# Kernel optimization log

Hardware: AMD Instinct MI355X
Metric: run time of the kernel (lower is better)

Reference implementation:

```python
import jax, jax.numpy as jnp
import numpy as np

B, N, D, E, H = 8, 2048, 256, 16, 8
CAP = max(min(N, int(N * 2.0 / E)), 4)  # eval capacity_factor = 2.0 -> 256
EPS = 1e-9
LOSS_COEF = 0.01


def _excl_cumsum(t, axis):
    return jnp.cumsum(t, axis=axis) - t


def _top2_gating(x, w_gating):
    # x: (B, N, D); w_gating: (D, E)
    raw = jax.nn.softmax(jnp.einsum('bnd,de->bne', x, w_gating), axis=-1)
    idx1 = jnp.argmax(raw, axis=-1)
    g1 = jnp.max(raw, axis=-1)
    m1 = jax.nn.one_hot(idx1, E, dtype=raw.dtype)
    gates2 = raw * (1.0 - m1)
    idx2 = jnp.argmax(gates2, axis=-1)
    g2 = jnp.max(gates2, axis=-1)
    m2 = jax.nn.one_hot(idx2, E, dtype=raw.dtype)
    denom = g1 + g2 + EPS
    g1 = g1 / denom
    g2 = g2 / denom
    # load-balance loss
    density_1 = m1.mean(axis=-2)          # (B, E)
    proxy = raw.mean(axis=-2)             # (B, E)
    loss = (proxy * density_1).mean() * float(E * E)
    # second policy == 'all': keep mask_2 as-is
    pos1 = _excl_cumsum(m1, -2) * m1
    m1 = m1 * (pos1 < float(CAP)).astype(m1.dtype)
    m1_count = m1.sum(axis=-2, keepdims=True)
    m1_flat = m1.sum(axis=-1)             # (B, N)
    pos1 = pos1.sum(axis=-1)              # (B, N)
    g1 = g1 * m1_flat
    pos2 = (_excl_cumsum(m2, -2) + m1_count) * m2
    m2 = m2 * (pos2 < float(CAP)).astype(m2.dtype)
    m2_flat = m2.sum(axis=-1)
    pos2 = pos2.sum(axis=-1)
    g2 = g2 * m2_flat
    oh_e1 = jax.nn.one_hot(idx1, E, dtype=raw.dtype)
    oh_e2 = jax.nn.one_hot(idx2, E, dtype=raw.dtype)
    oh_c1 = jax.nn.one_hot(pos1.astype(jnp.int32), CAP, dtype=raw.dtype)
    oh_c2 = jax.nn.one_hot(pos2.astype(jnp.int32), CAP, dtype=raw.dtype)
    # combine: (B, N, E, CAP); note torch applies mask_flat twice (idempotent)
    combine = ((g1 * m1_flat)[..., None, None] * oh_e1[..., :, None] * oh_c1[..., None, :]
               + (g2 * m2_flat)[..., None, None] * oh_e2[..., :, None] * oh_c2[..., None, :])
    dispatch = (combine > 0).astype(combine.dtype)
    return dispatch, combine, loss


def _mixer(xe, audio, Wq, Wkv, Wp, bp):
    # CrossModalMixer, eval mode (dropouts = identity)
    # xe: (B, CAP, D); audio: (B, 1, D)
    b, n, c = xe.shape
    dh = c // H
    scale = dh ** -0.5
    q = (audio @ Wq).reshape(b, 1, H, dh).transpose(0, 2, 1, 3)   # (b,h,1,dh)
    kv = (xe @ Wkv).reshape(b, n, 2, H, dh)
    k = kv[:, :, 0].transpose(0, 2, 1, 3)                          # (b,h,n,dh)
    v = kv[:, :, 1].transpose(0, 2, 1, 3)
    attn = jax.nn.softmax(jnp.einsum('bhqd,bhkd->bhqk', q, k) * scale, axis=-1)
    o = jnp.einsum('bhqk,bhkd->bhqd', attn, v).transpose(0, 2, 1, 3).reshape(b, 1, c)
    gate = jax.nn.sigmoid(o @ Wp + bp)                             # (b,1,c)
    return xe * gate                                               # einsum('bnc,bc->bnc')


def setup_inputs():
    ks = jax.random.split(jax.random.key(0), 7)
    return {
        'x': jax.random.normal(ks[0], (B, N, D), jnp.float32),
        'audio_feat': jax.random.normal(ks[1], (B, 1, D), jnp.float32),
        'w_gating': jax.random.normal(ks[2], (D, E), jnp.float32),
        'Wq': jax.random.normal(ks[3], (E, D, D), jnp.float32) * 0.02,
        'Wkv': jax.random.normal(ks[4], (E, D, 2 * D), jnp.float32) * 0.02,
        'Wp': jax.random.normal(ks[5], (E, D, D), jnp.float32) * 0.02,
        'bp': jnp.zeros((E, D), jnp.float32),
    }


def reference(x, audio_feat, w_gating, Wq, Wkv, Wp, bp):
    dispatch, combine, loss = _top2_gating(x, w_gating)
    expert_in = jnp.einsum('bnd,bnec->ebcd', x, dispatch)          # (E, B, CAP, D)
    outs = jax.vmap(_mixer, in_axes=(0, None, 0, 0, 0, 0))(expert_in, audio_feat, Wq, Wkv, Wp, bp)
    out = jnp.einsum('ebcd,bnec->bnd', outs, combine)
    return out, loss * LOSS_COEF
```

## Files before the change

### kernel.cpp

```cpp
#include <hip/hip_runtime.h>
#include <cstdint>
#include <cstddef>

#define BB 8
#define NN 2048
#define DD 256
#define EE 16
#define HH 8
#define CAPC 256
#define BN (BB*NN)
#define EB (EE*BB)

__global__ __launch_bounds__(256) void fused_gq_kernel(
    const float* __restrict__ x, const float* __restrict__ wg,
    const float* __restrict__ audio, const float* __restrict__ Wq,
    const float* __restrict__ Wkv,
    int* __restrict__ idx1a, int* __restrict__ idx2a,
    float* __restrict__ g1a, float* __restrict__ g2a,
    float* __restrict__ raw_part, float* __restrict__ cnt_part,
    float* __restrict__ rws)
{
  __shared__ union SM {
    struct { float wgS[DD*EE]; float lgp[4][64][17]; } g;
    struct { float aS[DD][8]; float qpart[8][32][9]; float qS[32][8];
             float wkS[DD][33]; } q;
  } sm;
  int tid = threadIdx.x;

  if (blockIdx.x < 256) {
    for (int t = tid; t < DD*EE; t += 256) sm.g.wgS[t] = wg[t];
    __syncthreads();
    int tk = tid & 63, kc = tid >> 6;
    int token0 = blockIdx.x * 64;
    int token = token0 + tk;
    const float4* xr = (const float4*)(x + (size_t)token*DD + kc*64);
    const float4* wg4 = (const float4*)sm.g.wgS;
    float lg[16];
#pragma unroll
    for (int e = 0; e < 16; ++e) lg[e] = 0.f;
#pragma unroll
    for (int d4 = 0; d4 < 16; ++d4) {
      float4 xv = xr[d4];
      float xa[4] = {xv.x, xv.y, xv.z, xv.w};
#pragma unroll
      for (int dd = 0; dd < 4; ++dd) {
        int d = kc*64 + d4*4 + dd;
        float xc = xa[dd];
#pragma unroll
        for (int j = 0; j < 4; ++j) {
          float4 w = wg4[d*4 + j];
          lg[4*j+0] += xc*w.x; lg[4*j+1] += xc*w.y;
          lg[4*j+2] += xc*w.z; lg[4*j+3] += xc*w.w;
        }
      }
    }
#pragma unroll
    for (int e = 0; e < 16; ++e) sm.g.lgp[kc][tk][e] = lg[e];
    __syncthreads();
    if (tid < 64) {
      int lane = tid;
      float l[16];
#pragma unroll
      for (int e = 0; e < 16; ++e)
        l[e] = sm.g.lgp[0][lane][e] + sm.g.lgp[1][lane][e]
             + sm.g.lgp[2][lane][e] + sm.g.lgp[3][lane][e];
      float mx = l[0];
#pragma unroll
      for (int e = 1; e < 16; ++e) mx = fmaxf(mx, l[e]);
      float p[16]; float s = 0.f;
#pragma unroll
      for (int e = 0; e < 16; ++e) { p[e] = expf(l[e] - mx); s += p[e]; }
      int i1 = 0; float b1 = p[0];
#pragma unroll
      for (int e = 1; e < 16; ++e) { if (p[e] > b1) { b1 = p[e]; i1 = e; } }
      float b2 = (i1 == 0) ? 0.f : p[0]; int i2 = 0;
#pragma unroll
      for (int e = 1; e < 16; ++e) { float v = (e == i1) ? 0.f : p[e]; if (v > b2) { b2 = v; i2 = e; } }
      float inv = 1.f / s;
      float g1 = b1*inv, g2 = b2*inv;
      float den = g1 + g2 + 1e-9f;
      g1 /= den; g2 /= den;
      int tok = token0 + lane;
      idx1a[tok] = i1; idx2a[tok] = i2;
      g1a[tok] = g1;   g2a[tok] = g2;
      int blk = blockIdx.x;
#pragma unroll
      for (int e = 0; e < 16; ++e) {
        float v = p[e] * inv;
        v += __shfl_down(v, 32); v += __shfl_down(v, 16);
        v += __shfl_down(v, 8);  v += __shfl_down(v, 4);
        v += __shfl_down(v, 2);  v += __shfl_down(v, 1);
        unsigned long long mb = __ballot(i1 == e);
        if (lane == 0) {
          raw_part[blk*16 + e] = v;
          cnt_part[blk*16 + e] = (float)__popcll(mb);
        }
      }
    }
  } else {
    int eh = blockIdx.x - 256;
    int e = eh >> 3, h = eh & 7;
    for (int i = tid; i < 2048; i += 256) { int b = i >> 8, k = i & 255; sm.q.aS[k][b] = audio[b*DD + k]; }
    __syncthreads();
    int j = tid & 31, kg = tid >> 5;
    const float* wq = Wq + (size_t)e*DD*DD + h*32 + j;
    float acc[8] = {0,0,0,0,0,0,0,0};
#pragma unroll
    for (int i = 0; i < 32; ++i) {
      int k = kg*32 + i;
      float w = wq[(size_t)k*DD];
      float4 a0 = *(const float4*)&sm.q.aS[k][0];
      float4 a1 = *(const float4*)&sm.q.aS[k][4];
      acc[0]+=w*a0.x; acc[1]+=w*a0.y; acc[2]+=w*a0.z; acc[3]+=w*a0.w;
      acc[4]+=w*a1.x; acc[5]+=w*a1.y; acc[6]+=w*a1.z; acc[7]+=w*a1.w;
    }
#pragma unroll
    for (int b = 0; b < 8; ++b) sm.q.qpart[kg][j][b] = acc[b];
    const float* wkbase = Wkv + (size_t)e*(DD*2*DD) + h*32;
    float4 stg[8];
#pragma unroll
    for (int m = 0; m < 8; ++m) {
      int row = m*32 + (tid >> 3), c4 = tid & 7;
      stg[m] = *(const float4*)(wkbase + (size_t)row*(2*DD) + c4*4);
    }
#pragma unroll
    for (int m = 0; m < 8; ++m) {
      int row = m*32 + (tid >> 3), c4 = tid & 7;
      sm.q.wkS[row][c4*4+0] = stg[m].x; sm.q.wkS[row][c4*4+1] = stg[m].y;
      sm.q.wkS[row][c4*4+2] = stg[m].z; sm.q.wkS[row][c4*4+3] = stg[m].w;
    }
    __syncthreads();
    {
      int jj = tid >> 3, b = tid & 7;
      float s = 0.f;
#pragma unroll
      for (int g = 0; g < 8; ++g) s += sm.q.qpart[g][jj][b];
      sm.q.qS[jj][b] = s;
    }
    __syncthreads();
    int d = tid;
    float racc[8] = {0,0,0,0,0,0,0,0};
#pragma unroll
    for (int jj = 0; jj < 32; ++jj) {
      float w = sm.q.wkS[d][jj];
      float4 q0 = *(const float4*)&sm.q.qS[jj][0];
      float4 q1 = *(const float4*)&sm.q.qS[jj][4];
      racc[0]+=w*q0.x; racc[1]+=w*q0.y; racc[2]+=w*q0.z; racc[3]+=w*q0.w;
      racc[4]+=w*q1.x; racc[5]+=w*q1.y; racc[6]+=w*q1.z; racc[7]+=w*q1.w;
    }
#pragma unroll
    for (int b = 0; b < 8; ++b)
      rws[((size_t)(e*8 + b))*2048 + d*8 + h] = racc[b];
  }
}

__global__ __launch_bounds__(256) void scan_kernel(
    const int* __restrict__ idx1a, const int* __restrict__ idx2a,
    float* __restrict__ g1a, float* __restrict__ g2a, int* __restrict__ slot_token,
    const float* __restrict__ raw_part, const float* __restrict__ cnt_part,
    float* __restrict__ out_loss)
{
  __shared__ unsigned long long m1s[16][32], m2s[16][32];
  __shared__ int wp1[16][32], wp2[16][32], mcnt[16];
  int b = blockIdx.x, tid = threadIdx.x;
  int wave = tid >> 6, lane = tid & 63;
  for (int i = tid; i < 16*CAPC; i += 256) {
    int e = i >> 8, s = i & 255;
    slot_token[(e*BB + b)*CAPC + s] = -1;
  }
  for (int w = wave; w < 32; w += 4) {
    int token = b*NN + w*64 + lane;
    int i1 = idx1a[token], i2 = idx2a[token];
#pragma unroll
    for (int e = 0; e < 16; ++e) {
      unsigned long long ma = __ballot(i1 == e);
      unsigned long long mb = __ballot(i2 == e);
      if (lane == 0) { m1s[e][w] = ma; m2s[e][w] = mb; }
    }
  }
  __syncthreads();
  if (tid < 16) {
    int run = 0;
    for (int w = 0; w < 32; ++w) { wp1[tid][w] = run; run += (int)__popcll(m1s[tid][w]); }
    mcnt[tid] = run < CAPC ? run : CAPC;
  } else if (tid < 32) {
    int e2 = tid - 16; int run = 0;
    for (int w = 0; w < 32; ++w) { wp2[e2][w] = run; run += (int)__popcll(m2s[e2][w]); }
  }
  __syncthreads();
  for (int w = wave; w < 32; w += 4) {
    int token = b*NN + w*64 + lane;
    int i1 = idx1a[token], i2 = idx2a[token];
    unsigned long long lt = (1ull << lane) - 1ull;
    int pos1 = wp1[i1][w] + (int)__popcll(m1s[i1][w] & lt);
    float g1 = g1a[token];
    bool k1 = pos1 < CAPC;
    g1a[token] = k1 ? g1 : 0.f;
    if (k1) slot_token[(i1*BB + b)*CAPC + pos1] = token;
    int pos2 = mcnt[i2] + wp2[i2][w] + (int)__popcll(m2s[i2][w] & lt);
    float g2 = g2a[token];
    bool k2 = pos2 < CAPC;
    g2a[token] = k2 ? g2 : 0.f;
    if (k2 && g2 > 0.f) slot_token[(i2*BB + b)*CAPC + pos2] = token;
  }
  if (blockIdx.x == 0) {
    float v = 0.f;
    if (tid < 128) {
      int bb = tid >> 4, e = tid & 15;
      float rs = 0.f, cs = 0.f;
#pragma unroll 4
      for (int k = 0; k < 32; ++k) {
        rs += raw_part[(bb*32 + k)*16 + e];
        cs += cnt_part[(bb*32 + k)*16 + e];
      }
      v = (rs * (1.f/(float)NN)) * (cs * (1.f/(float)NN));
    }
    v += __shfl_down(v, 32); v += __shfl_down(v, 16); v += __shfl_down(v, 8);
    v += __shfl_down(v, 4);  v += __shfl_down(v, 2);  v += __shfl_down(v, 1);
    __shared__ float r4[4];
    if ((tid & 63) == 0) r4[tid >> 6] = v;
    __syncthreads();
    if (tid == 0)
      out_loss[0] = (r4[0]+r4[1]+r4[2]+r4[3]) * ((float)(EE*EE) / (float)(BB*EE)) * 0.01f;
  }
}

__global__ __launch_bounds__(256) void lslotB_kernel(
    const float* __restrict__ x, const float* __restrict__ rws,
    const int* __restrict__ slot_token, float* __restrict__ lslot)
{
  __shared__ float rS[DD][8];
  __shared__ float lp[4][64][9];
  __shared__ int tokS[64];
  int tid = threadIdx.x;
  int eb = blockIdx.x >> 2, sc = blockIdx.x & 3;
  {
    const float4* rin = (const float4*)(rws + (size_t)eb*2048);
    float4* rS4 = (float4*)rS;
    rS4[tid] = rin[tid]; rS4[tid+256] = rin[tid+256];
  }
  if (tid < 64) tokS[tid] = slot_token[eb*CAPC + sc*64 + tid];
  __syncthreads();
  int s = tid >> 2, q = tid & 3;
  int token = tokS[s];
  float l[8] = {0,0,0,0,0,0,0,0};
  if (token >= 0) {
    const float4* xr = (const float4*)(x + (size_t)token*DD + q*64);
#pragma unroll
    for (int i = 0; i < 16; ++i) {
      float4 xv = xr[i];
      float xa[4] = {xv.x, xv.y, xv.z, xv.w};
#pragma unroll
      for (int dd = 0; dd < 4; ++dd) {
        int d = q*64 + i*4 + dd;
        float4 r0 = *(const float4*)&rS[d][0];
        float4 r1 = *(const float4*)&rS[d][4];
        float xc = xa[dd];
        l[0]+=xc*r0.x; l[1]+=xc*r0.y; l[2]+=xc*r0.z; l[3]+=xc*r0.w;
        l[4]+=xc*r1.x; l[5]+=xc*r1.y; l[6]+=xc*r1.z; l[7]+=xc*r1.w;
      }
    }
  }
#pragma unroll
  for (int h = 0; h < 8; ++h) lp[q][s][h] = l[h];
  __syncthreads();
#pragma unroll
  for (int r = 0; r < 2; ++r) {
    int o = tid*2 + r;
    int ss = o >> 3, h = o & 7;
    float v = (lp[0][ss][h] + lp[1][ss][h] + lp[2][ss][h] + lp[3][ss][h])
            * 0.17677669529663687f;
    lslot[((size_t)eb*CAPC + sc*64 + ss)*8 + h] = v;
  }
}

__global__ __launch_bounds__(256) void xattn_kernel(
    const float* __restrict__ x, const float* __restrict__ lslot,
    const int* __restrict__ slot_token, float* __restrict__ xattn)
{
  __shared__ float lS[CAPC][9];
  __shared__ float aS[HH][CAPC];
  __shared__ float part[4][HH][64];
  __shared__ int tokS[CAPC];
  __shared__ float red[16];
  int tid = threadIdx.x;
  int eb = blockIdx.x >> 2, dc = blockIdx.x & 3;
  int d0 = dc*64;
  {
    const float4* li = (const float4*)(lslot + (size_t)eb*CAPC*8);
    float4 v0 = li[tid*2], v1 = li[tid*2+1];
    lS[tid][0]=v0.x; lS[tid][1]=v0.y; lS[tid][2]=v0.z; lS[tid][3]=v0.w;
    lS[tid][4]=v1.x; lS[tid][5]=v1.y; lS[tid][6]=v1.z; lS[tid][7]=v1.w;
    tokS[tid] = slot_token[eb*CAPC + tid];
  }
  __syncthreads();
  int lane = tid & 63, wave = tid >> 6;
#pragma unroll
  for (int r = 0; r < 2; ++r) {
    int hh = wave + r*4;
    float m = fmaxf(fmaxf(lS[lane][hh], lS[lane+64][hh]),
                    fmaxf(lS[lane+128][hh], lS[lane+192][hh]));
    m = fmaxf(m, __shfl_down(m,32)); m = fmaxf(m, __shfl_down(m,16));
    m = fmaxf(m, __shfl_down(m,8));  m = fmaxf(m, __shfl_down(m,4));
    m = fmaxf(m, __shfl_down(m,2));  m = fmaxf(m, __shfl_down(m,1));
    if (lane == 0) red[hh] = m;
  }
  __syncthreads();
  float ex[8];
#pragma unroll
  for (int h = 0; h < 8; ++h) { ex[h] = expf(lS[tid][h] - red[h]); lS[tid][h] = ex[h]; }
  __syncthreads();
#pragma unroll
  for (int r = 0; r < 2; ++r) {
    int hh = wave + r*4;
    float s = lS[lane][hh] + lS[lane+64][hh] + lS[lane+128][hh] + lS[lane+192][hh];
    s += __shfl_down(s,32); s += __shfl_down(s,16); s += __shfl_down(s,8);
    s += __shfl_down(s,4);  s += __shfl_down(s,2);  s += __shfl_down(s,1);
    if (lane == 0) red[8+hh] = s;
  }
  __syncthreads();
#pragma unroll
  for (int h = 0; h < 8; ++h) aS[h][tid] = ex[h] / red[8+h];
  __syncthreads();
  int d = tid & 63, sc = tid >> 6;
  const float* xb = x + d0 + d;
  float acc[8] = {0,0,0,0,0,0,0,0};
#pragma unroll 4
  for (int i = 0; i < 64; ++i) {
    int s = sc*64 + i;
    int tk = tokS[s];
    int tkc = tk < 0 ? 0 : tk;
    float msk = tk < 0 ? 0.f : 1.f;
    float xv = xb[(size_t)tkc*DD] * msk;
#pragma unroll
    for (int h = 0; h < 8; ++h) acc[h] += aS[h][s] * xv;
  }
#pragma unroll
  for (int h = 0; h < 8; ++h) part[sc][h][d] = acc[h];
  __syncthreads();
#pragma unroll
  for (int r = 0; r < 2; ++r) {
    int o = r*256 + tid;
    int h = o >> 6, d2 = o & 63;
    float v = part[0][h][d2] + part[1][h][d2] + part[2][h][d2] + part[3][h][d2];
    xattn[(size_t)eb*2048 + h*DD + d0 + d2] = v;
  }
}

__global__ __launch_bounds__(256) void o_kernel(
    const float* __restrict__ xattn, const float* __restrict__ Wkv,
    float* __restrict__ o_ws)
{
  __shared__ float xaS[8][DD];
  __shared__ float op[8][32][9];
  int tid = threadIdx.x;
  int e = blockIdx.x >> 3, ch = blockIdx.x & 7;
  int c0 = ch*32, h = ch;
  for (int i = tid; i < 2048; i += 256) {
    int b = i >> 8, d = i & 255;
    xaS[b][d] = xattn[((size_t)(e*8 + b))*2048 + h*DD + d];
  }
  __syncthreads();
  int c = tid & 31, kc = tid >> 5;
  const float* wv = Wkv + (size_t)e*(DD*2*DD) + DD + c0 + c;
  float acc[8] = {0,0,0,0,0,0,0,0};
#pragma unroll
  for (int i = 0; i < 32; ++i) {
    int d = kc*32 + i;
    float w = wv[(size_t)d*(2*DD)];
#pragma unroll
    for (int b = 0; b < 8; ++b) acc[b] += w * xaS[b][d];
  }
#pragma unroll
  for (int b = 0; b < 8; ++b) op[kc][c][b] = acc[b];
  __syncthreads();
  int c2 = tid & 31, b2 = tid >> 5;
  float s = 0.f;
#pragma unroll
  for (int g = 0; g < 8; ++g) s += op[g][c2][b2];
  o_ws[((size_t)(e*8 + b2))*DD + c0 + c2] = s;
}

__global__ __launch_bounds__(256) void gate_kernel(
    const float* __restrict__ o_ws, const float* __restrict__ Wp,
    const float* __restrict__ bp, float* __restrict__ gateW)
{
  __shared__ float oS[8][DD];
  __shared__ float op[8][32][9];
  int tid = threadIdx.x;
  int e = blockIdx.x >> 3, ch = blockIdx.x & 7;
  int c0 = ch*32;
  for (int i = tid; i < 2048; i += 256) {
    int b = i >> 8, d = i & 255;
    oS[b][d] = o_ws[((size_t)(e*8 + b))*DD + d];
  }
  __syncthreads();
  int c = tid & 31, kc = tid >> 5;
  const float* wp = Wp + (size_t)e*DD*DD + c0 + c;
  float acc[8] = {0,0,0,0,0,0,0,0};
#pragma unroll
  for (int i = 0; i < 32; ++i) {
    int d = kc*32 + i;
    float w = wp[(size_t)d*DD];
#pragma unroll
    for (int b = 0; b < 8; ++b) acc[b] += w * oS[b][d];
  }
#pragma unroll
  for (int b = 0; b < 8; ++b) op[kc][c][b] = acc[b];
  __syncthreads();
  int c2 = tid & 31, b2 = tid >> 5;
  float s = bp[e*DD + c0 + c2];
#pragma unroll
  for (int g = 0; g < 8; ++g) s += op[g][c2][b2];
  gateW[((size_t)(e*8 + b2))*DD + c0 + c2] = 1.f / (1.f + expf(-s));
}

__global__ __launch_bounds__(256) void out_kernel(
    const float* __restrict__ x, const float* __restrict__ g1f, const float* __restrict__ g2f,
    const int* __restrict__ idx1a, const int* __restrict__ idx2a,
    const float* __restrict__ gateW, float* __restrict__ out)
{
  int idx = blockIdx.x*256 + threadIdx.x;
  int token = idx >> 6;
  int d4 = idx & 63;
  int b = token >> 11;
  float g1 = g1f[token], g2 = g2f[token];
  int e1 = idx1a[token], e2 = idx2a[token];
  float4 w1 = ((const float4*)(gateW + (size_t)(e1*BB+b)*DD))[d4];
  float4 w2 = ((const float4*)(gateW + (size_t)(e2*BB+b)*DD))[d4];
  float4 xv = ((const float4*)x)[idx];
  float4 o;
  o.x = xv.x*(g1*w1.x + g2*w2.x);
  o.y = xv.y*(g1*w1.y + g2*w2.y);
  o.z = xv.z*(g1*w1.z + g2*w2.z);
  o.w = xv.w*(g1*w1.w + g2*w2.w);
  ((float4*)out)[idx] = o;
}

extern "C" void kernel_launch(void* const* d_in, const int* in_sizes, int n_in,
                              void* d_out, int out_size, void* d_ws, size_t ws_size,
                              hipStream_t stream)
{
  const float* x     = (const float*)d_in[0];
  const float* audio = (const float*)d_in[1];
  const float* wg    = (const float*)d_in[2];
  const float* Wq    = (const float*)d_in[3];
  const float* Wkv   = (const float*)d_in[4];
  const float* Wp    = (const float*)d_in[5];
  const float* bp    = (const float*)d_in[6];
  float* out = (float*)d_out;

  float* raw_part = (float*)d_ws;
  float* cnt_part = raw_part + 256*16;
  int*   idx1a   = (int*)(cnt_part + 256*16);
  int*   idx2a   = idx1a + BN;
  float* g1a     = (float*)(idx2a + BN);
  float* g2a     = g1a + BN;
  int*   slot_token = (int*)(g2a + BN);
  float* rws     = (float*)(slot_token + EB*CAPC);
  float* lslot   = rws + (size_t)EB*2048;
  float* xattn   = lslot + (size_t)EB*CAPC*8;
  float* o_ws    = xattn + (size_t)EB*2048;
  float* gateW   = o_ws + (size_t)EB*DD;

  fused_gq_kernel<<<384, 256, 0, stream>>>(x, wg, audio, Wq, Wkv,
                                           idx1a, idx2a, g1a, g2a,
                                           raw_part, cnt_part, rws);
  scan_kernel<<<BB, 256, 0, stream>>>(idx1a, idx2a, g1a, g2a, slot_token,
                                      raw_part, cnt_part, out + (size_t)out_size - 1);
  lslotB_kernel<<<EB*4, 256, 0, stream>>>(x, rws, slot_token, lslot);
  xattn_kernel<<<EB*4, 256, 0, stream>>>(x, lslot, slot_token, xattn);
  o_kernel<<<EB, 256, 0, stream>>>(xattn, Wkv, o_ws);
  gate_kernel<<<EB, 256, 0, stream>>>(o_ws, Wp, bp, gateW);
  out_kernel<<<(BN*DD/4)/256, 256, 0, stream>>>(x, g1a, g2a, idx1a, idx2a, gateW, out);
}
```

Baseline: 155.6 us.

## Fuse per-expert attention, projection and gate kernels; prefetch weights during scan

Merges the four per-expert kernels (logit, attention-weighted sum, V projection, gate projection) into one 512-thread kernel per (expert,batch). The intermediate buffers and their global round trips go away, along with three launches. Extra blocks are added to the scan kernel that read all of Wkv and Wp to warm the cache while the scan runs. In exchange, the fused kernel launches only 128 blocks and each block now recomputes the V and Wp projections for a single batch. That multiplies weight reads by 8 compared with the earlier kernels, which shared each weight load across all 8 batches.

```diff
diff --git a/kernel.cpp b/kernel.cpp
--- a/kernel.cpp
+++ b/kernel.cpp
@@ -158,11 +158,26 @@
     const int* __restrict__ idx1a, const int* __restrict__ idx2a,
     float* __restrict__ g1a, float* __restrict__ g2a, int* __restrict__ slot_token,
     const float* __restrict__ raw_part, const float* __restrict__ cnt_part,
+    const float* __restrict__ Wkv, const float* __restrict__ Wp,
+    float* __restrict__ dummy,
     float* __restrict__ out_loss)
 {
+  int tid = threadIdx.x;
+  if (blockIdx.x >= BB) {
+    int pid = (blockIdx.x - BB)*256 + tid;
+    const float4* wk4 = (const float4*)Wkv;
+    const float4* wp4 = (const float4*)Wp;
+    float s = 0.f;
+    for (int i = pid; i < 786432; i += 56*256) {
+      float4 v = (i < 524288) ? wk4[i] : wp4[i - 524288];
+      s += v.x + v.y + v.z + v.w;
+    }
+    if (s != 0.f) dummy[pid & 1023] = s;
+    return;
+  }
   __shared__ unsigned long long m1s[16][32], m2s[16][32];
   __shared__ int wp1[16][32], wp2[16][32], mcnt[16];
-  int b = blockIdx.x, tid = threadIdx.x;
+  int b = blockIdx.x;
   int wave = tid >> 6, lane = tid & 63;
   for (int i = tid; i < 16*CAPC; i += 256) {
     int e = i >> 8, s = i & 255;
@@ -225,194 +240,145 @@
   }
 }
 
-__global__ __launch_bounds__(256) void lslotB_kernel(
+__global__ __launch_bounds__(512) void expert_kernel(
     const float* __restrict__ x, const float* __restrict__ rws,
-    const int* __restrict__ slot_token, float* __restrict__ lslot)
+    const int* __restrict__ slot_token, const float* __restrict__ Wkv,
+    const float* __restrict__ Wp, const float* __restrict__ bp,
+    float* __restrict__ gateW)
 {
   __shared__ float rS[DD][8];
-  __shared__ float lp[4][64][9];
-  __shared__ int tokS[64];
+  __shared__ int   tokS[CAPC];
+  __shared__ float lp[2][CAPC][9];
+  __shared__ float aST[CAPC][8];
+  __shared__ float part[2][8][DD];
+  __shared__ float xaS[8][DD];
+  __shared__ float oS[DD];
+  __shared__ float op[2][DD];
   int tid = threadIdx.x;
-  int eb = blockIdx.x >> 2, sc = blockIdx.x & 3;
+  int eb = blockIdx.x;
+  int e  = eb >> 3;
+
   {
     const float4* rin = (const float4*)(rws + (size_t)eb*2048);
-    float4* rS4 = (float4*)rS;
-    rS4[tid] = rin[tid]; rS4[tid+256] = rin[tid+256];
-  }
-  if (tid < 64) tokS[tid] = slot_token[eb*CAPC + sc*64 + tid];
-  __syncthreads();
-  int s = tid >> 2, q = tid & 3;
-  int token = tokS[s];
-  float l[8] = {0,0,0,0,0,0,0,0};
-  if (token >= 0) {
-    const float4* xr = (const float4*)(x + (size_t)token*DD + q*64);
-#pragma unroll
-    for (int i = 0; i < 16; ++i) {
-      float4 xv = xr[i];
-      float xa[4] = {xv.x, xv.y, xv.z, xv.w};
-#pragma unroll
-      for (int dd = 0; dd < 4; ++dd) {
-        int d = q*64 + i*4 + dd;
-        float4 r0 = *(const float4*)&rS[d][0];
-        float4 r1 = *(const float4*)&rS[d][4];
-        float xc = xa[dd];
-        l[0]+=xc*r0.x; l[1]+=xc*r0.y; l[2]+=xc*r0.z; l[3]+=xc*r0.w;
-        l[4]+=xc*r1.x; l[5]+=xc*r1.y; l[6]+=xc*r1.z; l[7]+=xc*r1.w;
+    ((float4*)rS)[tid] = rin[tid];
+    if (tid < CAPC) tokS[tid] = slot_token[eb*CAPC + tid];
+  }
+  __syncthreads();
+
+  {
+    int s = tid >> 1, q = tid & 1;
+    int token = tokS[s];
+    float l[8] = {0,0,0,0,0,0,0,0};
+    if (token >= 0) {
+      const float4* xr = (const float4*)(x + (size_t)token*DD) + q;
+#pragma unroll
+      for (int i = 0; i < 32; ++i) {
+        float4 xv = xr[i*2];
+        float xa[4] = {xv.x, xv.y, xv.z, xv.w};
+#pragma unroll
+        for (int dd = 0; dd < 4; ++dd) {
+          int d = i*8 + q*4 + dd;
+          float4 r0 = *(const float4*)&rS[d][0];
+          float4 r1 = *(const float4*)&rS[d][4];
+          float xc = xa[dd];
+          l[0]+=xc*r0.x; l[1]+=xc*r0.y; l[2]+=xc*r0.z; l[3]+=xc*r0.w;
+          l[4]+=xc*r1.x; l[5]+=xc*r1.y; l[6]+=xc*r1.z; l[7]+=xc*r1.w;
+        }
       }
     }
-  }
-#pragma unroll
-  for (int h = 0; h < 8; ++h) lp[q][s][h] = l[h];
-  __syncthreads();
-#pragma unroll
-  for (int r = 0; r < 2; ++r) {
-    int o = tid*2 + r;
-    int ss = o >> 3, h = o & 7;
-    float v = (lp[0][ss][h] + lp[1][ss][h] + lp[2][ss][h] + lp[3][ss][h])
-            * 0.17677669529663687f;
-    lslot[((size_t)eb*CAPC + sc*64 + ss)*8 + h] = v;
-  }
-}
-
-__global__ __launch_bounds__(256) void xattn_kernel(
-    const float* __restrict__ x, const float* __restrict__ lslot,
-    const int* __restrict__ slot_token, float* __restrict__ xattn)
-{
-  __shared__ float lS[CAPC][9];
-  __shared__ float aS[HH][CAPC];
-  __shared__ float part[4][HH][64];
-  __shared__ int tokS[CAPC];
-  __shared__ float red[16];
-  int tid = threadIdx.x;
-  int eb = blockIdx.x >> 2, dc = blockIdx.x & 3;
-  int d0 = dc*64;
-  {
-    const float4* li = (const float4*)(lslot + (size_t)eb*CAPC*8);
-    float4 v0 = li[tid*2], v1 = li[tid*2+1];
-    lS[tid][0]=v0.x; lS[tid][1]=v0.y; lS[tid][2]=v0.z; lS[tid][3]=v0.w;
-    lS[tid][4]=v1.x; lS[tid][5]=v1.y; lS[tid][6]=v1.z; lS[tid][7]=v1.w;
-    tokS[tid] = slot_token[eb*CAPC + tid];
-  }
-  __syncthreads();
-  int lane = tid & 63, wave = tid >> 6;
-#pragma unroll
-  for (int r = 0; r < 2; ++r) {
-    int hh = wave + r*4;
-    float m = fmaxf(fmaxf(lS[lane][hh], lS[lane+64][hh]),
-                    fmaxf(lS[lane+128][hh], lS[lane+192][hh]));
-    m = fmaxf(m, __shfl_down(m,32)); m = fmaxf(m, __shfl_down(m,16));
-    m = fmaxf(m, __shfl_down(m,8));  m = fmaxf(m, __shfl_down(m,4));
-    m = fmaxf(m, __shfl_down(m,2));  m = fmaxf(m, __shfl_down(m,1));
-    if (lane == 0) red[hh] = m;
-  }
-  __syncthreads();
-  float ex[8];
-#pragma unroll
-  for (int h = 0; h < 8; ++h) { ex[h] = expf(lS[tid][h] - red[h]); lS[tid][h] = ex[h]; }
-  __syncthreads();
-#pragma unroll
-  for (int r = 0; r < 2; ++r) {
-    int hh = wave + r*4;
-    float s = lS[lane][hh] + lS[lane+64][hh] + lS[lane+128][hh] + lS[lane+192][hh];
-    s += __shfl_down(s,32); s += __shfl_down(s,16); s += __shfl_down(s,8);
-    s += __shfl_down(s,4);  s += __shfl_down(s,2);  s += __shfl_down(s,1);
-    if (lane == 0) red[8+hh] = s;
-  }
-  __syncthreads();
-#pragma unroll
-  for (int h = 0; h < 8; ++h) aS[h][tid] = ex[h] / red[8+h];
-  __syncthreads();
-  int d = tid & 63, sc = tid >> 6;
-  const float* xb = x + d0 + d;
-  float acc[8] = {0,0,0,0,0,0,0,0};
+#pragma unroll
+    for (int h = 0; h < 8; ++h) lp[q][s][h] = l[h];
+  }
+  __syncthreads();
+#pragma unroll
+  for (int r = 0; r < 4; ++r) {
+    int idx = r*512 + tid;
+    int s2 = idx >> 3, h2 = idx & 7;
+    aST[s2][h2] = (lp[0][s2][h2] + lp[1][s2][h2]) * 0.17677669529663687f;
+  }
+  __syncthreads();
+
+  {
+    int wave = tid >> 6, lane = tid & 63;
+    int h = wave;
+    float v0 = aST[lane][h],     v1 = aST[lane+64][h];
+    float v2 = aST[lane+128][h], v3 = aST[lane+192][h];
+    float m = fmaxf(fmaxf(v0, v1), fmaxf(v2, v3));
+    m = fmaxf(m, __shfl_down(m, 32)); m = fmaxf(m, __shfl_down(m, 16));
+    m = fmaxf(m, __shfl_down(m, 8));  m = fmaxf(m, __shfl_down(m, 4));
+    m = fmaxf(m, __shfl_down(m, 2));  m = fmaxf(m, __shfl_down(m, 1));
+    m = __shfl(m, 0);
+    float e0 = expf(v0 - m), e1 = expf(v1 - m), e2 = expf(v2 - m), e3 = expf(v3 - m);
+    float sm = e0 + e1 + e2 + e3;
+    sm += __shfl_down(sm, 32); sm += __shfl_down(sm, 16); sm += __shfl_down(sm, 8);
+    sm += __shfl_down(sm, 4);  sm += __shfl_down(sm, 2);  sm += __shfl_down(sm, 1);
+    sm = __shfl(sm, 0);
+    float inv = 1.f / sm;
+    aST[lane][h]     = e0*inv; aST[lane+64][h]  = e1*inv;
+    aST[lane+128][h] = e2*inv; aST[lane+192][h] = e3*inv;
+  }
+  __syncthreads();
+
+  {
+    int d = tid & 255, sc = tid >> 8;
+    const float* xb = x + d;
+    float acc[8] = {0,0,0,0,0,0,0,0};
 #pragma unroll 4
-  for (int i = 0; i < 64; ++i) {
-    int s = sc*64 + i;
-    int tk = tokS[s];
-    int tkc = tk < 0 ? 0 : tk;
-    float msk = tk < 0 ? 0.f : 1.f;
-    float xv = xb[(size_t)tkc*DD] * msk;
-#pragma unroll
-    for (int h = 0; h < 8; ++h) acc[h] += aS[h][s] * xv;
-  }
-#pragma unroll
-  for (int h = 0; h < 8; ++h) part[sc][h][d] = acc[h];
-  __syncthreads();
-#pragma unroll
-  for (int r = 0; r < 2; ++r) {
-    int o = r*256 + tid;
-    int h = o >> 6, d2 = o & 63;
-    float v = part[0][h][d2] + part[1][h][d2] + part[2][h][d2] + part[3][h][d2];
-    xattn[(size_t)eb*2048 + h*DD + d0 + d2] = v;
-  }
-}
-
-__global__ __launch_bounds__(256) void o_kernel(
-    const float* __restrict__ xattn, const float* __restrict__ Wkv,
-    float* __restrict__ o_ws)
-{
-  __shared__ float xaS[8][DD];
-  __shared__ float op[8][32][9];
-  int tid = threadIdx.x;
-  int e = blockIdx.x >> 3, ch = blockIdx.x & 7;
-  int c0 = ch*32, h = ch;
-  for (int i = tid; i < 2048; i += 256) {
-    int b = i >> 8, d = i & 255;
-    xaS[b][d] = xattn[((size_t)(e*8 + b))*2048 + h*DD + d];
-  }
-  __syncthreads();
-  int c = tid & 31, kc = tid >> 5;
-  const float* wv = Wkv + (size_t)e*(DD*2*DD) + DD + c0 + c;
-  float acc[8] = {0,0,0,0,0,0,0,0};
-#pragma unroll
-  for (int i = 0; i < 32; ++i) {
-    int d = kc*32 + i;
-    float w = wv[(size_t)d*(2*DD)];
-#pragma unroll
-    for (int b = 0; b < 8; ++b) acc[b] += w * xaS[b][d];
-  }
-#pragma unroll
-  for (int b = 0; b < 8; ++b) op[kc][c][b] = acc[b];
-  __syncthreads();
-  int c2 = tid & 31, b2 = tid >> 5;
-  float s = 0.f;
-#pragma unroll
-  for (int g = 0; g < 8; ++g) s += op[g][c2][b2];
-  o_ws[((size_t)(e*8 + b2))*DD + c0 + c2] = s;
-}
-
-__global__ __launch_bounds__(256) void gate_kernel(
-    const float* __restrict__ o_ws, const float* __restrict__ Wp,
-    const float* __restrict__ bp, float* __restrict__ gateW)
-{
-  __shared__ float oS[8][DD];
-  __shared__ float op[8][32][9];
-  int tid = threadIdx.x;
-  int e = blockIdx.x >> 3, ch = blockIdx.x & 7;
-  int c0 = ch*32;
-  for (int i = tid; i < 2048; i += 256) {
-    int b = i >> 8, d = i & 255;
-    oS[b][d] = o_ws[((size_t)(e*8 + b))*DD + d];
-  }
-  __syncthreads();
-  int c = tid & 31, kc = tid >> 5;
-  const float* wp = Wp + (size_t)e*DD*DD + c0 + c;
-  float acc[8] = {0,0,0,0,0,0,0,0};
-#pragma unroll
-  for (int i = 0; i < 32; ++i) {
-    int d = kc*32 + i;
-    float w = wp[(size_t)d*DD];
-#pragma unroll
-    for (int b = 0; b < 8; ++b) acc[b] += w * oS[b][d];
-  }
-#pragma unroll
-  for (int b = 0; b < 8; ++b) op[kc][c][b] = acc[b];
-  __syncthreads();
-  int c2 = tid & 31, b2 = tid >> 5;
-  float s = bp[e*DD + c0 + c2];
-#pragma unroll
-  for (int g = 0; g < 8; ++g) s += op[g][c2][b2];
-  gateW[((size_t)(e*8 + b2))*DD + c0 + c2] = 1.f / (1.f + expf(-s));
+    for (int i = 0; i < 128; ++i) {
+      int s2 = sc*128 + i;
+      int tk = tokS[s2];
+      int tkc = tk < 0 ? 0 : tk;
+      float msk = tk < 0 ? 0.f : 1.f;
+      float xv = xb[(size_t)tkc*DD] * msk;
+      float4 a0 = *(const float4*)&aST[s2][0];
+      float4 a1 = *(const float4*)&aST[s2][4];
+      acc[0]+=a0.x*xv; acc[1]+=a0.y*xv; acc[2]+=a0.z*xv; acc[3]+=a0.w*xv;
+      acc[4]+=a1.x*xv; acc[5]+=a1.y*xv; acc[6]+=a1.z*xv; acc[7]+=a1.w*xv;
+    }
+#pragma unroll
+    for (int h = 0; h < 8; ++h) part[sc][h][d] = acc[h];
+  }
+  __syncthreads();
+#pragma unroll
+  for (int r = 0; r < 4; ++r) {
+    int idx = r*512 + tid;
+    int h2 = idx >> 8, d2 = idx & 255;
+    xaS[h2][d2] = part[0][h2][d2] + part[1][h2][d2];
+  }
+  __syncthreads();
+
+  {
+    int c = tid & 255, kc = tid >> 8;
+    int h = c >> 5;
+    const float* wv = Wkv + (size_t)e*(DD*2*DD) + DD + c;
+    float a = 0.f;
+#pragma unroll 8
+    for (int i = 0; i < 128; ++i) {
+      int d2 = kc*128 + i;
+      a += wv[(size_t)d2*(2*DD)] * xaS[h][d2];
+    }
+    op[kc][c] = a;
+  }
+  __syncthreads();
+  if (tid < DD) oS[tid] = op[0][tid] + op[1][tid];
+  __syncthreads();
+
+  {
+    int c = tid & 255, kc = tid >> 8;
+    const float* wp = Wp + (size_t)e*DD*DD + c;
+    float a = 0.f;
+#pragma unroll 8
+    for (int i = 0; i < 128; ++i) {
+      int d2 = kc*128 + i;
+      a += wp[(size_t)d2*DD] * oS[d2];
+    }
+    op[kc][c] = a;
+  }
+  __syncthreads();
+  if (tid < DD) {
+    float sv = bp[e*DD + tid] + op[0][tid] + op[1][tid];
+    gateW[(size_t)eb*DD + tid] = 1.f / (1.f + expf(-sv));
+  }
 }
 
 __global__ __launch_bounds__(256) void out_kernel(
@@ -458,19 +424,15 @@
   float* g2a     = g1a + BN;
   int*   slot_token = (int*)(g2a + BN);
   float* rws     = (float*)(slot_token + EB*CAPC);
-  float* lslot   = rws + (size_t)EB*2048;
-  float* xattn   = lslot + (size_t)EB*CAPC*8;
-  float* o_ws    = xattn + (size_t)EB*2048;
-  float* gateW   = o_ws + (size_t)EB*DD;
+  float* dummy   = rws + (size_t)EB*2048;
+  float* gateW   = dummy + 1024;
 
   fused_gq_kernel<<<384, 256, 0, stream>>>(x, wg, audio, Wq, Wkv,
                                            idx1a, idx2a, g1a, g2a,
                                            raw_part, cnt_part, rws);
-  scan_kernel<<<BB, 256, 0, stream>>>(idx1a, idx2a, g1a, g2a, slot_token,
-                                      raw_part, cnt_part, out + (size_t)out_size - 1);
-  lslotB_kernel<<<EB*4, 256, 0, stream>>>(x, rws, slot_token, lslot);
-  xattn_kernel<<<EB*4, 256, 0, stream>>>(x, lslot, slot_token, xattn);
-  o_kernel<<<EB, 256, 0, stream>>>(xattn, Wkv, o_ws);
-  gate_kernel<<<EB, 256, 0, stream>>>(o_ws, Wp, bp, gateW);
+  scan_kernel<<<64, 256, 0, stream>>>(idx1a, idx2a, g1a, g2a, slot_token,
+                                      raw_part, cnt_part, Wkv, Wp, dummy,
+                                      out + (size_t)out_size - 1);
+  expert_kernel<<<EB, 512, 0, stream>>>(x, rws, slot_token, Wkv, Wp, bp, gateW);
   out_kernel<<<(BN*DD/4)/256, 256, 0, stream>>>(x, g1a, g2a, idx1a, idx2a, gateW, out);
 }
```

Measured after the change: 153.3 us. No clear change (-1.5%).
